# Kernel optimization log

Measured on AMD Instinct MI355X. Metric: run time of the kernel, lower is better.

The kernel has to match this reference:

```python
import jax, jax.numpy as jnp
import numpy as np

B, N, T, NUM_API = 4, 160, 512, 20000  # queries, list length, tag vocab size, number of APIs
TAG_DENSITY = 0.05


def _compute_lambda(y_score, tag_set, M):
    # y_score: [N]; tag_set: [N,T] multi-hot rows api_tag_embedding[y_pred]; M: [T] multi-hot target.
    # Faithful to mode == 'cover' branch of LambdaRankLoss.compute_lambda.
    n = tag_set.shape[0]
    f32 = tag_set.dtype
    idx = jnp.arange(n)
    log_values = jnp.log2(jnp.arange(2, n + 2, dtype=f32))             # [N]
    P = jax.lax.cummax(tag_set, axis=0)                                # set_union_list = cummax(tag_set) [N,T]
    Mc = (jnp.count_nonzero(M) + 1).astype(f32)                        # M_nonzero_count
    # count_nonzero(clamp(M - set_union_list[k], min=0)) == #(M_t > P[k,t])
    cU = jnp.sum(M[None, :] > P, axis=1).astype(f32)                   # [N]

    # pre[i] = rowwise-max of tag_set[:i-1]. Torch quirk: i==0 -> tag_set[:-1] (all but last row); i==1 -> empty.
    pre = jnp.where(idx[:, None] == 0, P[n - 2][None, :],
                    jnp.where(idx[:, None] == 1, jnp.zeros((), f32),
                              P[jnp.clip(idx - 2, 0, n - 1)]))         # [N,T] (0 is max-identity: entries >= 0)

    # R[a,b] = max(tag_set[a..b]) along rows; 0 when b < a (rows before a masked to 0, then cummax)
    masked = jnp.where(idx[None, :, None] >= idx[:, None, None], tag_set[None, :, :], jnp.zeros((), f32))
    R = jax.lax.cummax(masked, axis=1)                                 # [N,N,T]

    # mid[k,i] = max(tag_set[i+1:k]) = R[i+1, k-1] when k >= i+2, else empty -> 0
    i_ix = idx[None, :]
    k_ix = idx[:, None]
    mid = jnp.where((k_ix >= i_ix + 2)[:, :, None],
                    R[jnp.clip(i_ix + 1, 0, n - 1), jnp.clip(k_ix - 1, 0, n - 1)],
                    jnp.zeros((), f32))                                # [K,I,T]

    # A[k,i] = max(cat(tag_set[:i-1], tag_set[i+1:k]));  Q[k,i,j] = max(A[k,i], tag_set[j])
    A = jnp.maximum(pre[None, :, :], mid)                              # [K,I,T]
    # count_nonzero(clamp(M - Q[k,i,j], 0)) = sum_t [M_t > A[k,i,t]] * [M_t > tag_set[j,t]]
    aM = (M[None, None, :] > A).astype(f32)                            # [K,I,T]
    bM = (M[None, :] > tag_set).astype(f32)                            # [J,T]
    cQ = jnp.einsum('kit,jt->kij', aM, bM)                             # [K,I,J] Q_nonzero counts

    W = (cU[:, None, None] - cQ) / (Mc * log_values[:, None, None])    # [K,I,J]
    # Z1[i,j] = sum_{k=i}^{j-1} W[k,i,j]  (strictly upper-triangular in (i,j))
    maskZ = (idx[None, :, None] <= idx[:, None, None]) & (idx[:, None, None] < idx[None, None, :])
    Z1 = jnp.sum(jnp.where(maskZ, W, jnp.zeros((), f32)), axis=0)      # [I,J]

    # lambda1[i,j] = 1 / (1 + exp(s_i - s_j))
    lam = 1.0 / (1.0 + jnp.exp(y_score[:, None] - y_score[None, :]))
    return jnp.sum(lam * Z1) / jnp.asarray(n + 1, f32)


def setup_inputs() -> dict:
    key = jax.random.key(0)
    k1, k2, k3, k4 = jax.random.split(key, 4)
    y_scores = jax.random.normal(k1, (B, N), jnp.float32)
    y_preds = jax.random.randint(k2, (B, N), 0, NUM_API)
    M = (jax.random.uniform(k3, (B, T)) < TAG_DENSITY).astype(jnp.float32)
    api_tag_embedding = (jax.random.uniform(k4, (NUM_API, T)) < TAG_DENSITY).astype(jnp.float32)
    return {"y_scores": y_scores, "M": M, "api_tag_embedding": api_tag_embedding, "y_preds": y_preds}


def reference(y_scores, M, api_tag_embedding, y_preds):
    def per_query(s, m, pred):
        return _compute_lambda(s, api_tag_embedding[pred], m)
    vals = jax.vmap(per_query)(y_scores, M, y_preds)  # [B]
    return jnp.mean(vals)  # loss / len(y_scores)
```

## Files before the change

kernel.cpp:

```cpp
#include <hip/hip_runtime.h>
#include <stdint.h>

typedef unsigned long long u64;

constexpr int B_ = 4;
constexpr int N_ = 160;
constexpr int T_ = 512;
constexpr int W_ = T_ / 64;

__global__ __launch_bounds__(64) void pack_tags(const float* __restrict__ emb,
                                                const int* __restrict__ preds,
                                                u64* __restrict__ tags) {
    int row  = blockIdx.x;
    int lane = threadIdx.x;
    const float* src = emb + (long long)preds[row] * T_;
#pragma unroll
    for (int w = 0; w < W_; ++w) {
        float v = src[w * 64 + lane];
        u64 m = __ballot(v != 0.0f);
        if (lane == 0) tags[(long long)row * W_ + w] = m;
    }
}

__global__ __launch_bounds__(256) void pack_scan(const float* __restrict__ Mf,
                                                 const u64* __restrict__ tags,
                                                 u64* __restrict__ Mp,
                                                 u64* __restrict__ P,
                                                 float* __restrict__ cU,
                                                 float* __restrict__ Mc) {
    __shared__ u64 S0[N_ * W_];
    __shared__ u64 S1[N_ * W_];
    __shared__ u64 Msh[W_];

    const int b    = blockIdx.x;
    const int tid  = threadIdx.x;
    const int lane = tid & 63;
    const int wv   = tid >> 6;

    for (int w = wv; w < W_; w += 4) {
        float v = Mf[(long long)b * T_ + w * 64 + lane];
        u64 m = __ballot(v != 0.0f);
        if (lane == 0) { Msh[w] = m; Mp[b * W_ + w] = m; }
    }
    for (int x = tid; x < N_ * W_; x += 256)
        S0[x] = tags[(long long)b * N_ * W_ + x];
    __syncthreads();

    u64* src = S0;
    u64* dst = S1;
    for (int d = 1; d < N_; d <<= 1) {
        for (int x = tid; x < N_ * W_; x += 256) {
            int r = x >> 3;
            u64 v = src[x];
            if (r >= d) v |= src[x - d * W_];
            dst[x] = v;
        }
        __syncthreads();
        u64* t = src; src = dst; dst = t;
    }

    for (int x = tid; x < N_ * W_; x += 256)
        P[(long long)b * N_ * W_ + x] = src[x];

    if (tid < N_) {
        int c = 0;
#pragma unroll
        for (int w = 0; w < W_; ++w)
            c += __popcll(Msh[w] & ~src[tid * W_ + w]);
        cU[b * N_ + tid] = (float)c;
    }
    if (tid == 0) {
        int c = 0;
#pragma unroll
        for (int w = 0; w < W_; ++w) c += __popcll(Msh[w]);
        Mc[b] = (float)(c + 1);
    }
}

__global__ __launch_bounds__(256) void lambda_main(const u64* __restrict__ tags,
                                                   const u64* __restrict__ Mp,
                                                   const u64* __restrict__ P,
                                                   const float* __restrict__ cU,
                                                   const float* __restrict__ Mc,
                                                   const float* __restrict__ scores,
                                                   double* __restrict__ partials) {
    constexpr int LD = N_ + 1;
    __shared__ u64 tagsT[W_ * LD];
    __shared__ u64 bufA[W_ * LD];
    __shared__ u64 bufB[W_ * LD];
    __shared__ u64 awT[W_ * LD];
    __shared__ u64 bT[W_ * LD];
    __shared__ u64 Msh[W_];
    __shared__ float scoresL[N_];
    __shared__ float redF[4];

    const int k   = blockIdx.x;
    const int b   = blockIdx.y;
    const int tid = threadIdx.x;

    if (tid < W_)  Msh[tid]    = Mp[b * W_ + tid];
    if (tid < N_)  scoresL[tid] = scores[b * N_ + tid];

    for (int x = tid; x < W_ * N_; x += 256) {
        int r = x >> 3, w = x & 7;
        tagsT[w * LD + r] = tags[(long long)b * N_ * W_ + x];
    }
    __syncthreads();

    for (int x = tid; x < W_ * N_; x += 256) {
        int r = x >> 3, w = x & 7;
        bufA[w * LD + r] = (r < k) ? tagsT[w * LD + r] : 0ull;
    }
    __syncthreads();

    u64* src = bufA;
    u64* dst = bufB;
    for (int d = 1; d < N_; d <<= 1) {
        for (int x = tid; x < W_ * N_; x += 256) {
            int r = x >> 3, w = x & 7;
            u64 v = src[w * LD + r];
            if (r + d < k) v |= src[w * LD + r + d];
            dst[w * LD + r] = v;
        }
        __syncthreads();
        u64* t = src; src = dst; dst = t;
    }

    for (int x = tid; x < W_ * N_; x += 256) {
        int i = x >> 3, w = x & 7;
        u64 pre;
        if (i == 1) pre = 0ull;
        else {
            int sr = (i == 0) ? (N_ - 2) : (i - 2);
            pre = P[((long long)b * N_ + sr) * W_ + w];
        }
        u64 sv = (i + 1 < k) ? src[w * LD + i + 1] : 0ull;
        awT[w * LD + i] = Msh[w] & ~pre & ~sv;
        bT[w * LD + i]  = Msh[w] & ~tagsT[w * LD + i];
    }
    __syncthreads();

    const int m = N_ - 1 - k;
    float accLam = 0.0f, accC = 0.0f;
    if (m > 0) {
        const int npairs = (k + 1) * m;
        if (tid < npairs) {
            int cnt = (npairs - tid + 255) >> 8;
            int i   = tid / m;
            int jj  = tid - i * m;
            const int di = 256 / m;
            const int rj = 256 - di * m;
            for (int c = 0; c < cnt; ++c) {
                const int j = k + 1 + jj;
                int cc = 0;
#pragma unroll
                for (int w = 0; w < W_; ++w)
                    cc += __popcll(awT[w * LD + i] & bT[w * LD + j]);
                float lam = 1.0f / (1.0f + __expf(scoresL[i] - scoresL[j]));
                accLam += lam;
                accC   += lam * (float)cc;
                i += di; jj += rj;
                if (jj >= m) { jj -= m; ++i; }
            }
        }
    }

    const float cUk = cU[b * N_ + k];
    float val = cUk * accLam - accC;
    for (int off = 32; off >= 1; off >>= 1) val += __shfl_down(val, off, 64);
    if ((tid & 63) == 0) redF[tid >> 6] = val;
    __syncthreads();
    if (tid == 0) {
        float s = redF[0] + redF[1] + redF[2] + redF[3];
        float invlog = 1.0f / log2f((float)(k + 2));
        partials[b * N_ + k] = (double)(s * invlog) / (double)Mc[b];
    }
}

__global__ __launch_bounds__(256) void finalize(const double* __restrict__ partials,
                                                float* __restrict__ out) {
    __shared__ double redD[4];
    const int tid = threadIdx.x;
    double s = 0.0;
    for (int x = tid; x < B_ * N_; x += 256) s += partials[x];
    for (int off = 32; off >= 1; off >>= 1) s += __shfl_down(s, off, 64);
    if ((tid & 63) == 0) redD[tid >> 6] = s;
    __syncthreads();
    if (tid == 0) {
        double t = redD[0] + redD[1] + redD[2] + redD[3];
        out[0] = (float)(t / ((double)(N_ + 1) * (double)B_));
    }
}

extern "C" void kernel_launch(void* const* d_in, const int* in_sizes, int n_in,
                              void* d_out, int out_size, void* d_ws, size_t ws_size,
                              hipStream_t stream) {
    const float* y_scores = (const float*)d_in[0];
    const float* Mf       = (const float*)d_in[1];
    const float* emb      = (const float*)d_in[2];
    const int*   preds    = (const int*)d_in[3];
    float* out = (float*)d_out;

    u64* tags = (u64*)d_ws;
    u64* P    = tags + (size_t)B_ * N_ * W_;
    u64* Mp   = P + (size_t)B_ * N_ * W_;
    double* partials = (double*)(Mp + B_ * W_);
    float* cU = (float*)(partials + B_ * N_);
    float* Mc = cU + B_ * N_;

    pack_tags<<<B_ * N_, 64, 0, stream>>>(emb, preds, tags);
    pack_scan<<<B_, 256, 0, stream>>>(Mf, tags, Mp, P, cU, Mc);
    dim3 grid(N_, B_);
    lambda_main<<<grid, 256, 0, stream>>>(tags, Mp, P, cU, Mc, y_scores, partials);
    finalize<<<1, 256, 0, stream>>>(partials, out);
}
```

Baseline: 113.1 us.

## Fuse finalize into lambda_main, trim suffix scan, and map threads to j

```diff
diff --git a/kernel.cpp b/kernel.cpp
--- a/kernel.cpp
+++ b/kernel.cpp
@@ -10,9 +10,11 @@
 
 __global__ __launch_bounds__(64) void pack_tags(const float* __restrict__ emb,
                                                 const int* __restrict__ preds,
-                                                u64* __restrict__ tags) {
+                                                u64* __restrict__ tags,
+                                                int* __restrict__ counter) {
     int row  = blockIdx.x;
     int lane = threadIdx.x;
+    if (row == 0 && lane == 0) *counter = 0;
     const float* src = emb + (long long)preds[row] * T_;
 #pragma unroll
     for (int w = 0; w < W_; ++w) {
@@ -77,56 +79,52 @@
     }
 }
 
-__global__ __launch_bounds__(256) void lambda_main(const u64* __restrict__ tags,
+__global__ __launch_bounds__(192) void lambda_main(const u64* __restrict__ tags,
                                                    const u64* __restrict__ Mp,
                                                    const u64* __restrict__ P,
                                                    const float* __restrict__ cU,
                                                    const float* __restrict__ Mc,
                                                    const float* __restrict__ scores,
-                                                   double* __restrict__ partials) {
-    constexpr int LD = N_ + 1;
-    __shared__ u64 tagsT[W_ * LD];
-    __shared__ u64 bufA[W_ * LD];
-    __shared__ u64 bufB[W_ * LD];
-    __shared__ u64 awT[W_ * LD];
-    __shared__ u64 bT[W_ * LD];
+                                                   double* __restrict__ partials,
+                                                   int* __restrict__ counter,
+                                                   float* __restrict__ out) {
+    __shared__ u64 tagsL[N_ * W_];
+    __shared__ u64 S0[N_ * W_];
+    __shared__ u64 S1[N_ * W_];
     __shared__ u64 Msh[W_];
     __shared__ float scoresL[N_];
-    __shared__ float redF[4];
+    __shared__ float redF[3];
+    __shared__ int isLast;
+    __shared__ double redD[3];
 
     const int k   = blockIdx.x;
     const int b   = blockIdx.y;
     const int tid = threadIdx.x;
 
-    if (tid < W_)  Msh[tid]    = Mp[b * W_ + tid];
-    if (tid < N_)  scoresL[tid] = scores[b * N_ + tid];
-
-    for (int x = tid; x < W_ * N_; x += 256) {
-        int r = x >> 3, w = x & 7;
-        tagsT[w * LD + r] = tags[(long long)b * N_ * W_ + x];
-    }
-    __syncthreads();
-
-    for (int x = tid; x < W_ * N_; x += 256) {
-        int r = x >> 3, w = x & 7;
-        bufA[w * LD + r] = (r < k) ? tagsT[w * LD + r] : 0ull;
-    }
-    __syncthreads();
-
-    u64* src = bufA;
-    u64* dst = bufB;
-    for (int d = 1; d < N_; d <<= 1) {
-        for (int x = tid; x < W_ * N_; x += 256) {
-            int r = x >> 3, w = x & 7;
-            u64 v = src[w * LD + r];
-            if (r + d < k) v |= src[w * LD + r + d];
-            dst[w * LD + r] = v;
+    if (tid < W_) Msh[tid] = Mp[b * W_ + tid];
+    for (int x = tid; x < N_; x += 192) scoresL[x] = scores[b * N_ + x];
+    for (int x = tid; x < N_ * W_; x += 192)
+        tagsL[x] = tags[(long long)b * N_ * W_ + x];
+    __syncthreads();
+
+    const int ne = k * W_;
+    u64* src = S0;
+    u64* dst = S1;
+    for (int x = tid; x < ne; x += 192) src[x] = tagsL[x];
+    __syncthreads();
+    for (int d = 1; d < k; d <<= 1) {
+        for (int x = tid; x < ne; x += 192) {
+            int r = x >> 3;
+            u64 v = src[x];
+            if (r + d < k) v |= src[x + d * W_];
+            dst[x] = v;
         }
         __syncthreads();
         u64* t = src; src = dst; dst = t;
     }
 
-    for (int x = tid; x < W_ * N_; x += 256) {
+    u64* awL = dst;
+    for (int x = tid; x < (k + 1) * W_; x += 192) {
         int i = x >> 3, w = x & 7;
         u64 pre;
         if (i == 1) pre = 0ull;
@@ -134,61 +132,57 @@
             int sr = (i == 0) ? (N_ - 2) : (i - 2);
             pre = P[((long long)b * N_ + sr) * W_ + w];
         }
-        u64 sv = (i + 1 < k) ? src[w * LD + i + 1] : 0ull;
-        awT[w * LD + i] = Msh[w] & ~pre & ~sv;
-        bT[w * LD + i]  = Msh[w] & ~tagsT[w * LD + i];
+        u64 sv = (i + 1 < k) ? src[(i + 1) * W_ + w] : 0ull;
+        awL[x] = Msh[w] & ~pre & ~sv;
     }
     __syncthreads();
 
     const int m = N_ - 1 - k;
-    float accLam = 0.0f, accC = 0.0f;
-    if (m > 0) {
-        const int npairs = (k + 1) * m;
-        if (tid < npairs) {
-            int cnt = (npairs - tid + 255) >> 8;
-            int i   = tid / m;
-            int jj  = tid - i * m;
-            const int di = 256 / m;
-            const int rj = 256 - di * m;
-            for (int c = 0; c < cnt; ++c) {
-                const int j = k + 1 + jj;
-                int cc = 0;
-#pragma unroll
-                for (int w = 0; w < W_; ++w)
-                    cc += __popcll(awT[w * LD + i] & bT[w * LD + j]);
-                float lam = 1.0f / (1.0f + __expf(scoresL[i] - scoresL[j]));
-                accLam += lam;
-                accC   += lam * (float)cc;
-                i += di; jj += rj;
-                if (jj >= m) { jj -= m; ++i; }
-            }
-        }
-    }
-
-    const float cUk = cU[b * N_ + k];
-    float val = cUk * accLam - accC;
+    float val = 0.0f;
+    if (tid < m) {
+        const int j = k + 1 + tid;
+        u64 Bw[W_];
+#pragma unroll
+        for (int w = 0; w < W_; ++w) Bw[w] = Msh[w] & ~tagsL[j * W_ + w];
+        const float sj  = scoresL[j];
+        const float cUk = cU[b * N_ + k];
+        float accLam = 0.0f, accC = 0.0f;
+#pragma unroll 4
+        for (int i = 0; i <= k; ++i) {
+            int cc = 0;
+#pragma unroll
+            for (int w = 0; w < W_; ++w)
+                cc += __popcll(awL[i * W_ + w] & Bw[w]);
+            float lam = 1.0f / (1.0f + __expf(scoresL[i] - sj));
+            accLam += lam;
+            accC   += lam * (float)cc;
+        }
+        val = cUk * accLam - accC;
+    }
     for (int off = 32; off >= 1; off >>= 1) val += __shfl_down(val, off, 64);
     if ((tid & 63) == 0) redF[tid >> 6] = val;
     __syncthreads();
     if (tid == 0) {
-        float s = redF[0] + redF[1] + redF[2] + redF[3];
+        float s = redF[0] + redF[1] + redF[2];
         float invlog = 1.0f / log2f((float)(k + 2));
         partials[b * N_ + k] = (double)(s * invlog) / (double)Mc[b];
-    }
-}
-
-__global__ __launch_bounds__(256) void finalize(const double* __restrict__ partials,
-                                                float* __restrict__ out) {
-    __shared__ double redD[4];
-    const int tid = threadIdx.x;
-    double s = 0.0;
-    for (int x = tid; x < B_ * N_; x += 256) s += partials[x];
-    for (int off = 32; off >= 1; off >>= 1) s += __shfl_down(s, off, 64);
-    if ((tid & 63) == 0) redD[tid >> 6] = s;
-    __syncthreads();
-    if (tid == 0) {
-        double t = redD[0] + redD[1] + redD[2] + redD[3];
-        out[0] = (float)(t / ((double)(N_ + 1) * (double)B_));
+        __threadfence();
+        int done = atomicAdd(counter, 1);
+        isLast = (done == N_ * B_ - 1) ? 1 : 0;
+    }
+    __syncthreads();
+
+    if (isLast) {
+        __threadfence();
+        double s = 0.0;
+        for (int x = tid; x < B_ * N_; x += 192) s += partials[x];
+        for (int off = 32; off >= 1; off >>= 1) s += __shfl_down(s, off, 64);
+        if ((tid & 63) == 0) redD[tid >> 6] = s;
+        __syncthreads();
+        if (tid == 0) {
+            double t = redD[0] + redD[1] + redD[2];
+            out[0] = (float)(t / ((double)(N_ + 1) * (double)B_));
+        }
     }
 }
 
@@ -207,10 +201,11 @@
     double* partials = (double*)(Mp + B_ * W_);
     float* cU = (float*)(partials + B_ * N_);
     float* Mc = cU + B_ * N_;
-
-    pack_tags<<<B_ * N_, 64, 0, stream>>>(emb, preds, tags);
+    int* counter = (int*)(Mc + B_);
+
+    pack_tags<<<B_ * N_, 64, 0, stream>>>(emb, preds, tags, counter);
     pack_scan<<<B_, 256, 0, stream>>>(Mf, tags, Mp, P, cU, Mc);
     dim3 grid(N_, B_);
-    lambda_main<<<grid, 256, 0, stream>>>(tags, Mp, P, cU, Mc, y_scores, partials);
-    finalize<<<1, 256, 0, stream>>>(partials, out);
-}
+    lambda_main<<<grid, 192, 0, stream>>>(tags, Mp, P, cU, Mc, y_scores,
+                                          partials, counter, out);
+}
```

Measured after the change: 131.7 us. +16.5%, slower.

## Precompute A-masks incrementally in pack_scan, fuse finalize via last-block atomic

Applied to the files above, without the earlier changes.

```diff
diff --git a/kernel.cpp b/kernel.cpp
--- a/kernel.cpp
+++ b/kernel.cpp
@@ -7,12 +7,15 @@
 constexpr int N_ = 160;
 constexpr int T_ = 512;
 constexpr int W_ = T_ / 64;
+constexpr int LDP_ = N_ + 1;
 
 __global__ __launch_bounds__(64) void pack_tags(const float* __restrict__ emb,
                                                 const int* __restrict__ preds,
-                                                u64* __restrict__ tags) {
+                                                u64* __restrict__ tags,
+                                                int* __restrict__ counter) {
     int row  = blockIdx.x;
     int lane = threadIdx.x;
+    if (row == 0 && lane == 0) *counter = 0;
     const float* src = emb + (long long)preds[row] * T_;
 #pragma unroll
     for (int w = 0; w < W_; ++w) {
@@ -25,9 +28,9 @@
 __global__ __launch_bounds__(256) void pack_scan(const float* __restrict__ Mf,
                                                  const u64* __restrict__ tags,
                                                  u64* __restrict__ Mp,
-                                                 u64* __restrict__ P,
                                                  float* __restrict__ cU,
-                                                 float* __restrict__ Mc) {
+                                                 float* __restrict__ Mc,
+                                                 u64* __restrict__ AW) {
     __shared__ u64 S0[N_ * W_];
     __shared__ u64 S1[N_ * W_];
     __shared__ u64 Msh[W_];
@@ -59,9 +62,6 @@
         u64* t = src; src = dst; dst = t;
     }
 
-    for (int x = tid; x < N_ * W_; x += 256)
-        P[(long long)b * N_ * W_ + x] = src[x];
-
     if (tid < N_) {
         int c = 0;
 #pragma unroll
@@ -75,74 +75,98 @@
         for (int w = 0; w < W_; ++w) c += __popcll(Msh[w]);
         Mc[b] = (float)(c + 1);
     }
+
+    u64* tg = dst;
+    for (int x = tid; x < N_ * W_; x += 256)
+        tg[x] = tags[(long long)b * N_ * W_ + x];
+    __syncthreads();
+
+    if (tid < N_) {
+        const int i = tid;
+        u64 aw[W_];
+#pragma unroll
+        for (int w = 0; w < W_; ++w) {
+            u64 pre;
+            if (i == 1) pre = 0ull;
+            else {
+                int sr = (i == 0) ? (N_ - 2) : (i - 2);
+                pre = src[sr * W_ + w];
+            }
+            aw[w] = Msh[w] & ~pre;
+        }
+        for (int k = 0; k < N_; ++k) {
+            if (k >= i) {
+                u64* dstp = AW + (((long long)b * N_ + k) * N_ + i) * W_;
+#pragma unroll
+                for (int w = 0; w < W_; ++w) dstp[w] = aw[w];
+                if (k > i) {
+#pragma unroll
+                    for (int w = 0; w < W_; ++w) aw[w] &= ~tg[k * W_ + w];
+                }
+            }
+        }
+    }
 }
 
 __global__ __launch_bounds__(256) void lambda_main(const u64* __restrict__ tags,
                                                    const u64* __restrict__ Mp,
-                                                   const u64* __restrict__ P,
+                                                   const u64* __restrict__ AW,
                                                    const float* __restrict__ cU,
                                                    const float* __restrict__ Mc,
                                                    const float* __restrict__ scores,
-                                                   double* __restrict__ partials) {
-    constexpr int LD = N_ + 1;
-    __shared__ u64 tagsT[W_ * LD];
-    __shared__ u64 bufA[W_ * LD];
-    __shared__ u64 bufB[W_ * LD];
-    __shared__ u64 awT[W_ * LD];
-    __shared__ u64 bT[W_ * LD];
-    __shared__ u64 Msh[W_];
+                                                   double* __restrict__ partials,
+                                                   int* __restrict__ counter,
+                                                   float* __restrict__ out) {
+    __shared__ u64 awL[W_ * LDP_];
+    __shared__ u64 bLT[W_ * LDP_];
     __shared__ float scoresL[N_];
     __shared__ float redF[4];
+    __shared__ double redD[4];
+    __shared__ int isLast;
 
     const int k   = blockIdx.x;
     const int b   = blockIdx.y;
     const int tid = threadIdx.x;
-
-    if (tid < W_)  Msh[tid]    = Mp[b * W_ + tid];
-    if (tid < N_)  scoresL[tid] = scores[b * N_ + tid];
-
-    for (int x = tid; x < W_ * N_; x += 256) {
+    const int m   = N_ - 1 - k;
+
+    u64 Mr[W_];
+#pragma unroll
+    for (int w = 0; w < W_; ++w) Mr[w] = Mp[b * W_ + w];
+
+    for (int x = tid; x < N_; x += 256) scoresL[x] = scores[b * N_ + x];
+
+    const u64* AWk = AW + ((long long)b * N_ + k) * N_ * W_;
+    for (int x = tid; x < (k + 1) * W_; x += 256) {
         int r = x >> 3, w = x & 7;
-        tagsT[w * LD + r] = tags[(long long)b * N_ * W_ + x];
-    }
-    __syncthreads();
-
-    for (int x = tid; x < W_ * N_; x += 256) {
-        int r = x >> 3, w = x & 7;
-        bufA[w * LD + r] = (r < k) ? tagsT[w * LD + r] : 0ull;
-    }
-    __syncthreads();
-
-    u64* src = bufA;
-    u64* dst = bufB;
-    for (int d = 1; d < N_; d <<= 1) {
-        for (int x = tid; x < W_ * N_; x += 256) {
-            int r = x >> 3, w = x & 7;
-            u64 v = src[w * LD + r];
-            if (r + d < k) v |= src[w * LD + r + d];
-            dst[w * LD + r] = v;
-        }
-        __syncthreads();
-        u64* t = src; src = dst; dst = t;
-    }
-
-    for (int x = tid; x < W_ * N_; x += 256) {
-        int i = x >> 3, w = x & 7;
-        u64 pre;
-        if (i == 1) pre = 0ull;
-        else {
-            int sr = (i == 0) ? (N_ - 2) : (i - 2);
-            pre = P[((long long)b * N_ + sr) * W_ + w];
-        }
-        u64 sv = (i + 1 < k) ? src[w * LD + i + 1] : 0ull;
-        awT[w * LD + i] = Msh[w] & ~pre & ~sv;
-        bT[w * LD + i]  = Msh[w] & ~tagsT[w * LD + i];
-    }
-    __syncthreads();
-
-    const int m = N_ - 1 - k;
+        awL[w * LDP_ + r] = AWk[x];
+    }
+    for (int x = tid; x < m * W_; x += 256) {
+        int j = k + 1 + (x >> 3), w = x & 7;
+        bLT[w * LDP_ + j] = Mr[w] & ~tags[((long long)b * N_ + j) * W_ + w];
+    }
+    __syncthreads();
+
+    const float cUk = cU[b * N_ + k];
     float accLam = 0.0f, accC = 0.0f;
-    if (m > 0) {
+
+    if (m >= 64) {
+        if (tid < m) {
+            const int j = k + 1 + tid;
+            u64 Bw[W_];
+#pragma unroll
+            for (int w = 0; w < W_; ++w) Bw[w] = bLT[w * LDP_ + j];
+            const float sj = scoresL[j];
+            for (int i = 0; i <= k; ++i) {
+                int cc = 0;
+#pragma unroll
+                for (int w = 0; w < W_; ++w)
+                    cc += __popcll(awL[w * LDP_ + i] & Bw[w]);
+                float lam = 1.0f / (1.0f + __expf(scoresL[i] - sj));
+                accLam += lam;
+                accC   += lam * (float)cc;
+            }
+        }
+    } else if (m > 0) {
         const int npairs = (k + 1) * m;
         if (tid < npairs) {
             int cnt = (npairs - tid + 255) >> 8;
@@ -155,7 +179,7 @@
                 int cc = 0;
 #pragma unroll
                 for (int w = 0; w < W_; ++w)
-                    cc += __popcll(awT[w * LD + i] & bT[w * LD + j]);
+                    cc += __popcll(awL[w * LDP_ + i] & bLT[w * LDP_ + j]);
                 float lam = 1.0f / (1.0f + __expf(scoresL[i] - scoresL[j]));
                 accLam += lam;
                 accC   += lam * (float)cc;
@@ -165,7 +189,6 @@
         }
     }
 
-    const float cUk = cU[b * N_ + k];
     float val = cUk * accLam - accC;
     for (int off = 32; off >= 1; off >>= 1) val += __shfl_down(val, off, 64);
     if ((tid & 63) == 0) redF[tid >> 6] = val;
@@ -174,21 +197,23 @@
         float s = redF[0] + redF[1] + redF[2] + redF[3];
         float invlog = 1.0f / log2f((float)(k + 2));
         partials[b * N_ + k] = (double)(s * invlog) / (double)Mc[b];
-    }
-}
-
-__global__ __launch_bounds__(256) void finalize(const double* __restrict__ partials,
-                                                float* __restrict__ out) {
-    __shared__ double redD[4];
-    const int tid = threadIdx.x;
-    double s = 0.0;
-    for (int x = tid; x < B_ * N_; x += 256) s += partials[x];
-    for (int off = 32; off >= 1; off >>= 1) s += __shfl_down(s, off, 64);
-    if ((tid & 63) == 0) redD[tid >> 6] = s;
-    __syncthreads();
-    if (tid == 0) {
-        double t = redD[0] + redD[1] + redD[2] + redD[3];
-        out[0] = (float)(t / ((double)(N_ + 1) * (double)B_));
+        __threadfence();
+        int done = atomicAdd(counter, 1);
+        isLast = (done == N_ * B_ - 1) ? 1 : 0;
+    }
+    __syncthreads();
+
+    if (isLast) {
+        __threadfence();
+        double s = 0.0;
+        for (int x = tid; x < B_ * N_; x += 256) s += partials[x];
+        for (int off = 32; off >= 1; off >>= 1) s += __shfl_down(s, off, 64);
+        if ((tid & 63) == 0) redD[tid >> 6] = s;
+        __syncthreads();
+        if (tid == 0) {
+            double t = redD[0] + redD[1] + redD[2] + redD[3];
+            out[0] = (float)(t / ((double)(N_ + 1) * (double)B_));
+        }
     }
 }
 
@@ -202,15 +227,16 @@
     float* out = (float*)d_out;
 
     u64* tags = (u64*)d_ws;
-    u64* P    = tags + (size_t)B_ * N_ * W_;
-    u64* Mp   = P + (size_t)B_ * N_ * W_;
-    double* partials = (double*)(Mp + B_ * W_);
+    u64* Mp   = tags + (size_t)B_ * N_ * W_;
+    u64* AW   = Mp + (size_t)B_ * W_;
+    double* partials = (double*)(AW + (size_t)B_ * N_ * N_ * W_);
     float* cU = (float*)(partials + B_ * N_);
     float* Mc = cU + B_ * N_;
-
-    pack_tags<<<B_ * N_, 64, 0, stream>>>(emb, preds, tags);
-    pack_scan<<<B_, 256, 0, stream>>>(Mf, tags, Mp, P, cU, Mc);
+    int* counter = (int*)(Mc + B_);
+
+    pack_tags<<<B_ * N_, 64, 0, stream>>>(emb, preds, tags, counter);
+    pack_scan<<<B_, 256, 0, stream>>>(Mf, tags, Mp, cU, Mc, AW);
     dim3 grid(N_, B_);
-    lambda_main<<<grid, 256, 0, stream>>>(tags, Mp, P, cU, Mc, y_scores, partials);
-    finalize<<<1, 256, 0, stream>>>(partials, out);
-}
+    lambda_main<<<grid, 256, 0, stream>>>(tags, Mp, AW, cU, Mc, y_scores,
+                                          partials, counter, out);
+}
```

Result: slower. 141.2 us (+24.9%).
